# Optimization experiments

Measured on AMD Instinct MI355X. Metric: run time of the kernel, lower is better.

The kernel has to match this reference:

```python
import jax, jax.numpy as jnp
import numpy as np

N_NODES = 100000
N_EDGES = 1600000
IN_DIM = 128      # 1 (degree) + 127 (raw feat)
HID = 128
N_GRAPHS = 100


def setup_inputs() -> dict:
    key = jax.random.key(0)
    ks = jax.random.split(key, 16)
    feat = jax.random.normal(ks[0], (N_NODES, IN_DIM - 1), dtype=jnp.float32)
    src = jax.random.randint(ks[1], (N_EDGES,), 0, N_NODES, dtype=jnp.int32)
    dst = jax.random.randint(ks[2], (N_EDGES,), 0, N_NODES, dtype=jnp.int32)
    graph_ids = jnp.sort(jax.random.randint(ks[3], (N_NODES,), 0, N_GRAPHS, dtype=jnp.int32))
    s = 1.0 / np.sqrt(IN_DIM)
    W0 = jax.random.uniform(ks[4], (HID, IN_DIM), jnp.float32, -s, s)
    b0 = jax.random.uniform(ks[5], (HID,), jnp.float32, -s, s)
    s = 1.0 / np.sqrt(HID)
    W1 = jax.random.uniform(ks[6], (HID, HID), jnp.float32, -s, s)
    b1 = jax.random.uniform(ks[7], (HID,), jnp.float32, -s, s)
    W2 = jax.random.uniform(ks[8], (HID, HID), jnp.float32, -s, s)
    b2 = jax.random.uniform(ks[9], (HID,), jnp.float32, -s, s)
    Wc1 = jax.random.uniform(ks[10], (HID, HID), jnp.float32, -s, s)
    bc1 = jax.random.uniform(ks[11], (HID,), jnp.float32, -s, s)
    Wc2 = jax.random.uniform(ks[12], (1, HID), jnp.float32, -s, s)
    bc2 = jax.random.uniform(ks[13], (1,), jnp.float32, -s, s)
    return {"feat": feat, "src": src, "dst": dst, "graph_ids": graph_ids,
            "num_graphs": N_GRAPHS,
            "W0": W0, "b0": b0, "W1": W1, "b1": b1, "W2": W2, "b2": b2,
            "Wc1": Wc1, "bc1": bc1, "Wc2": Wc2, "bc2": bc2}


def _gcn_layer(h, src, dst, deg, W, b):
    # mean over in-neighbor messages; zero-in-degree nodes keep old h (DGL reduce never fires)
    n = h.shape[0]
    summed = jax.ops.segment_sum(h[src], dst, num_segments=n)  # [N, d]
    mean = summed / jnp.maximum(deg, 1.0)[:, None]
    agg = jnp.where((deg > 0)[:, None], mean, h)
    return jax.nn.relu(agg @ W.T + b)


def reference(feat, src, dst, graph_ids, num_graphs,
              W0, b0, W1, b1, W2, b2, Wc1, bc1, Wc2, bc2):
    n = feat.shape[0]
    deg = jax.ops.segment_sum(jnp.ones(src.shape[0], jnp.float32), dst, num_segments=n)  # in-degrees
    h = jnp.concatenate([deg[:, None], feat], axis=-1)  # [N, IN_DIM]
    for W, b in ((W0, b0), (W1, b1), (W2, b2)):
        h = _gcn_layer(h, src, dst, deg, W, b)
    # dgl.mean_nodes: per-graph mean of node features
    counts = jax.ops.segment_sum(jnp.ones(n, jnp.float32), graph_ids, num_segments=num_graphs)
    hg = jax.ops.segment_sum(h, graph_ids, num_segments=num_graphs) / jnp.maximum(counts, 1.0)[:, None]
    # faithful: classify1 applied twice, no activation (F.relu was passed as bias flag)
    hg = hg @ Wc1.T + bc1
    hg = hg @ Wc1.T + bc1
    hg = hg @ Wc2.T + bc2
    return hg  # [num_graphs, 1]
```

## Files before the change

### kernel.cpp

```cpp
#include <hip/hip_runtime.h>
#include <hip/hip_bf16.h>

#define HID 128
#define NRAW 127
#define BSH 8
#define BNODES 256
#define APAD 68


typedef __attribute__((ext_vector_type(8))) short short8;
typedef __attribute__((ext_vector_type(4))) float floatx4;
typedef __attribute__((ext_vector_type(2))) float floatx2;

__device__ inline unsigned pack_bf2(float x, float y) {
    unsigned bx = __float_as_uint(x);
    unsigned by = __float_as_uint(y);
    bx += 0x7fffu + ((bx >> 16) & 1u);
    by += 0x7fffu + ((by >> 16) & 1u);
    return (bx >> 16) | (by & 0xffff0000u);
}
__device__ inline float bf_lo(unsigned u) { return __uint_as_float(u << 16); }
__device__ inline float bf_hi(unsigned u) { return __uint_as_float(u & 0xffff0000u); }


__global__ void init_kernel(const float* __restrict__ W0, const float* __restrict__ W1,
                            const float* __restrict__ W2, const float* __restrict__ Wc1,
                            unsigned* __restrict__ O0, unsigned* __restrict__ O1,
                            unsigned* __restrict__ O2, float* __restrict__ Wc1p,
                            int* __restrict__ gbucket, float* __restrict__ hg,
                            float* __restrict__ counts, int G) {
    int id = blockIdx.x * blockDim.x + threadIdx.x;
    if (id < 512) gbucket[id] = 0;
    if (id < G * HID) hg[id] = 0.f;
    if (id < G) counts[id] = 0.f;
    if (id < 16384) {
        int t = id >> 7, p = id & 127;
        Wc1p[id] = Wc1[t * 128 + ((p & 7) * 16 + (p >> 3))];
    }
    if (id < 3 * 8192) {
        int sel = id >> 13, l = id & 8191;
        const float* W = sel == 0 ? W0 : (sel == 1 ? W1 : W2);
        unsigned* O = sel == 0 ? O0 : (sel == 1 ? O1 : O2);
        int o = l >> 6, pp = (l & 63) * 2;
        int k0 = (pp & 7) * 16 + (pp >> 3);
        int k1 = ((pp + 1) & 7) * 16 + ((pp + 1) >> 3);
        O[l] = pack_bf2(W[o * 128 + k0], W[o * 128 + k1]);
    }
}


__global__ __launch_bounds__(256) void bucket_count_kernel(const int* __restrict__ dst,
                                                           int* __restrict__ gbucket,
                                                           int E, int NB) {
    __shared__ int hist[512];
    int t = threadIdx.x;
    for (int b = t; b < NB; b += 256) hist[b] = 0;
    __syncthreads();
    int base = blockIdx.x * 4096;
    #pragma unroll
    for (int j = 0; j < 16; ++j) {
        int e = base + j * 256 + t;
        if (e < E) atomicAdd(&hist[dst[e] >> BSH], 1);
    }
    __syncthreads();
    for (int b = t; b < NB; b += 256) {
        int v = hist[b];
        if (v) atomicAdd(&gbucket[b], v);
    }
}

__global__ void bucket_scan_kernel(const int* __restrict__ gbucket, int* __restrict__ bstart,
                                   int* __restrict__ gcur, int NB, int E) {
    __shared__ int sm[512];
    int t = threadIdx.x;
    int v = (t < NB) ? gbucket[t] : 0;
    sm[t] = v;
    __syncthreads();
    for (int off = 1; off < 512; off <<= 1) {
        int add = (t >= off) ? sm[t - off] : 0;
        __syncthreads();
        sm[t] += add;
        __syncthreads();
    }
    if (t < NB) {
        int ex = sm[t] - v;
        bstart[t] = ex;
        gcur[t] = ex;
    }
    if (t == 0) bstart[NB] = E;
}

__global__ __launch_bounds__(256) void bucket_scatter_kernel(const int* __restrict__ src,
                                                             const int* __restrict__ dst,
                                                             int* __restrict__ gcur,
                                                             uint2* __restrict__ staging,
                                                             int E, int NB) {
    __shared__ int hist[512];
    __shared__ int base[512];
    int t = threadIdx.x;
    for (int b = t; b < NB; b += 256) hist[b] = 0;
    __syncthreads();
    int s[16], d[16], r[16];
    int e0 = blockIdx.x * 4096;
    #pragma unroll
    for (int j = 0; j < 16; ++j) {
        int e = e0 + j * 256 + t;
        if (e < E) {
            s[j] = src[e];
            d[j] = dst[e];
            r[j] = atomicAdd(&hist[d[j] >> BSH], 1);
        } else d[j] = -1;
    }
    __syncthreads();
    for (int b = t; b < NB; b += 256) {
        int v = hist[b];
        base[b] = v ? atomicAdd(&gcur[b], v) : 0;
    }
    __syncthreads();
    #pragma unroll
    for (int j = 0; j < 16; ++j) {
        if (d[j] >= 0) {
            int b = d[j] >> BSH;
            staging[base[b] + r[j]] = make_uint2((unsigned)s[j], (unsigned)d[j]);
        }
    }
}

__global__ __launch_bounds__(256) void csr_build_kernel(const uint2* __restrict__ staging,
                                                        const int* __restrict__ bstart,
                                                        int* __restrict__ rp, int* __restrict__ csr,
                                                        float* __restrict__ degf,
                                                        int N, int E, int NB) {
    __shared__ int hist[256];
    __shared__ int sm[256];
    __shared__ int excl[256];
    __shared__ int cnt[256];
    int t = threadIdx.x;
    int b = blockIdx.x;
    int nbase = b << BSH;
    int s0 = bstart[b], e1 = bstart[b + 1];
    hist[t] = 0;
    __syncthreads();
    for (int i = s0 + t; i < e1; i += 256) {
        uint2 p = staging[i];
        atomicAdd(&hist[p.y & (BNODES - 1)], 1);
    }
    __syncthreads();
    int h = hist[t];
    sm[t] = h;
    __syncthreads();
    for (int off = 1; off < 256; off <<= 1) {
        int add = (t >= off) ? sm[t - off] : 0;
        __syncthreads();
        sm[t] += add;
        __syncthreads();
    }
    excl[t] = sm[t] - h;
    cnt[t] = 0;
    int n = nbase + t;
    if (n < N) {
        rp[n] = s0 + (sm[t] - h);
        degf[n] = (float)h;
    }
    if (b == NB - 1 && t == 0) rp[N] = E;
    __syncthreads();
    for (int i = s0 + t; i < e1; i += 256) {
        uint2 p = staging[i];
        int dl = p.y & (BNODES - 1);
        int pos = s0 + excl[dl] + atomicAdd(&cnt[dl], 1);
        csr[pos] = (int)p.x;
    }
}


__global__ void build_h0_kernel(const float* __restrict__ feat,
                                unsigned* __restrict__ h8, int N) {
    int id = blockIdx.x * blockDim.x + threadIdx.x;
    if (id >= N * 32) return;
    int n = id >> 5, c = id & 31;
    const float* fr = feat + (size_t)n * NRAW;
    int base = c >> 1, hb = (c & 1) * 4;
    float f[4];
    #pragma unroll
    for (int j = 0; j < 4; ++j) {
        int l = (hb + j) * 16 + base;
        f[j] = (l == 0) ? 0.f : fr[l - 1];
    }
    unsigned w = __builtin_amdgcn_cvt_pk_fp8_f32(f[0], f[1], 0, false);
    w = __builtin_amdgcn_cvt_pk_fp8_f32(f[2], f[3], w, true);
    h8[id] = w;
}


__global__ __launch_bounds__(256) void agg_fp8_kernel(const unsigned* __restrict__ h8,
                                                      unsigned* __restrict__ agg,
                                                      const int* __restrict__ rp,
                                                      const int* __restrict__ csr,
                                                      const float* __restrict__ degf, int N) {
    int t = threadIdx.x;
    int col = t & 15;
    int i = blockIdx.x * 16 + (t >> 4);
    if (i >= N) return;
    int start = rp[i], end = rp[i + 1];
    int deg = end - start;
    const uint2* h2 = (const uint2*)h8;
    if (deg == 0) {
        uint2 v = h2[(size_t)i * 16 + col];
        floatx2 l0 = __builtin_amdgcn_cvt_pk_f32_fp8(v.x, false);
        floatx2 h0 = __builtin_amdgcn_cvt_pk_f32_fp8(v.x, true);
        floatx2 l1 = __builtin_amdgcn_cvt_pk_f32_fp8(v.y, false);
        floatx2 h1 = __builtin_amdgcn_cvt_pk_f32_fp8(v.y, true);
        uint4 r;
        r.x = pack_bf2(l0[0], l0[1]);
        r.y = pack_bf2(h0[0], h0[1]);
        r.z = pack_bf2(l1[0], l1[1]);
        r.w = pack_bf2(h1[0], h1[1]);
        ((uint4*)agg)[(size_t)i * 16 + col] = r;
        return;
    }
    floatx2 a0 = {0.f, 0.f}, a1 = {0.f, 0.f}, a2 = {0.f, 0.f}, a3 = {0.f, 0.f};
    float dsum = 0.f;
    int p = start;
    for (; p + 4 <= end; p += 4) {
        int i0 = csr[p];
        int i1 = csr[p + 1];
        int i2 = csr[p + 2];
        int i3 = csr[p + 3];
        uint2 v0 = h2[(size_t)i0 * 16 + col];
        uint2 v1 = h2[(size_t)i1 * 16 + col];
        uint2 v2 = h2[(size_t)i2 * 16 + col];
        uint2 v3 = h2[(size_t)i3 * 16 + col];
        if (degf && col == 0) dsum += degf[i0] + degf[i1] + degf[i2] + degf[i3];
        a0 += __builtin_amdgcn_cvt_pk_f32_fp8(v0.x, false);
        a1 += __builtin_amdgcn_cvt_pk_f32_fp8(v0.x, true);
        a2 += __builtin_amdgcn_cvt_pk_f32_fp8(v0.y, false);
        a3 += __builtin_amdgcn_cvt_pk_f32_fp8(v0.y, true);
        a0 += __builtin_amdgcn_cvt_pk_f32_fp8(v1.x, false);
        a1 += __builtin_amdgcn_cvt_pk_f32_fp8(v1.x, true);
        a2 += __builtin_amdgcn_cvt_pk_f32_fp8(v1.y, false);
        a3 += __builtin_amdgcn_cvt_pk_f32_fp8(v1.y, true);
        a0 += __builtin_amdgcn_cvt_pk_f32_fp8(v2.x, false);
        a1 += __builtin_amdgcn_cvt_pk_f32_fp8(v2.x, true);
        a2 += __builtin_amdgcn_cvt_pk_f32_fp8(v2.y, false);
        a3 += __builtin_amdgcn_cvt_pk_f32_fp8(v2.y, true);
        a0 += __builtin_amdgcn_cvt_pk_f32_fp8(v3.x, false);
        a1 += __builtin_amdgcn_cvt_pk_f32_fp8(v3.x, true);
        a2 += __builtin_amdgcn_cvt_pk_f32_fp8(v3.y, false);
        a3 += __builtin_amdgcn_cvt_pk_f32_fp8(v3.y, true);
    }
    for (; p < end; ++p) {
        int i0 = csr[p];
        uint2 v0 = h2[(size_t)i0 * 16 + col];
        if (degf && col == 0) dsum += degf[i0];
        a0 += __builtin_amdgcn_cvt_pk_f32_fp8(v0.x, false);
        a1 += __builtin_amdgcn_cvt_pk_f32_fp8(v0.x, true);
        a2 += __builtin_amdgcn_cvt_pk_f32_fp8(v0.y, false);
        a3 += __builtin_amdgcn_cvt_pk_f32_fp8(v0.y, true);
    }
    if (degf && col == 0) a0[0] = dsum;
    float inv = 1.f / (float)deg;
    uint4 r;
    r.x = pack_bf2(a0[0] * inv, a0[1] * inv);
    r.y = pack_bf2(a1[0] * inv, a1[1] * inv);
    r.z = pack_bf2(a2[0] * inv, a2[1] * inv);
    r.w = pack_bf2(a3[0] * inv, a3[1] * inv);
    ((uint4*)agg)[(size_t)i * 16 + col] = r;
}


__global__ __launch_bounds__(256) void mfma_gemm_kernel(const unsigned* __restrict__ A,
                                                        unsigned* __restrict__ out8,
                                                        unsigned* __restrict__ outb,
                                                        const unsigned* __restrict__ Wb,
                                                        const float* __restrict__ bias, int N) {
    __shared__ unsigned Al[64 * APAD];
    int t = threadIdx.x;
    int n0 = blockIdx.x * 64;
    #pragma unroll
    for (int c = 0; c < 4; ++c) {
        int f = c * 256 + t;
        int row = f >> 4, c4 = f & 15;
        int n = n0 + row;
        uint4 v = make_uint4(0u, 0u, 0u, 0u);
        if (n < N) v = ((const uint4*)A)[(size_t)n * 16 + c4];
        *(uint4*)&Al[row * APAD + c4 * 4] = v;
    }
    __syncthreads();

    int wv = t >> 6, lane = t & 63;
    int m = lane & 15, q = lane >> 4;
    floatx4 acc[8];
    #pragma unroll
    for (int ot = 0; ot < 8; ++ot) acc[ot] = (floatx4)(0.f);

    #pragma unroll
    for (int kt = 0; kt < 4; ++kt) {
        short8 af = *(const short8*)&Al[(wv * 16 + m) * APAD + kt * 16 + q * 4];
        short8 bf[8];
        #pragma unroll
        for (int ot = 0; ot < 8; ++ot)
            bf[ot] = *(const short8*)&Wb[(ot * 16 + m) * 64 + kt * 16 + q * 4];
        #pragma unroll
        for (int ot = 0; ot < 8; ++ot)
            acc[ot] = __builtin_amdgcn_mfma_f32_16x16x32_bf16(af, bf[ot], acc[ot], 0, 0, 0);
    }

    float bv[8];
    #pragma unroll
    for (int ot = 0; ot < 8; ++ot) bv[ot] = bias[ot * 16 + m];

    #pragma unroll
    for (int r = 0; r < 4; ++r) {
        int n = n0 + wv * 16 + q * 4 + r;
        if (n < N) {
            float vv[8];
            #pragma unroll
            for (int ot = 0; ot < 8; ++ot) vv[ot] = fmaxf(acc[ot][r] + bv[ot], 0.f);
            if (out8) {
                unsigned w0 = __builtin_amdgcn_cvt_pk_fp8_f32(vv[0], vv[1], 0, false);
                w0 = __builtin_amdgcn_cvt_pk_fp8_f32(vv[2], vv[3], w0, true);
                unsigned w1 = __builtin_amdgcn_cvt_pk_fp8_f32(vv[4], vv[5], 0, false);
                w1 = __builtin_amdgcn_cvt_pk_fp8_f32(vv[6], vv[7], w1, true);
                ((uint2*)out8)[(size_t)n * 16 + m] = make_uint2(w0, w1);
            }
            if (outb) {
                uint4 w;
                w.x = pack_bf2(vv[0], vv[1]);
                w.y = pack_bf2(vv[2], vv[3]);
                w.z = pack_bf2(vv[4], vv[5]);
                w.w = pack_bf2(vv[6], vv[7]);
                ((uint4*)outb)[(size_t)n * 16 + m] = w;
            }
        }
    }
}


__global__ __launch_bounds__(256) void pool_kernel(const unsigned* __restrict__ h,
                                                   const int* __restrict__ gid,
                                                   float* __restrict__ hg,
                                                   float* __restrict__ counts, int N) {
    int c = threadIdx.x & 63;
    int q = threadIdx.x >> 6;
    int n0 = blockIdx.x * 64;
    int nend = min(n0 + 64, N);
    float ax = 0.f, ay = 0.f, cnt = 0.f;
    int cur = -1;
    for (int n = n0 + q; n < nend; n += 4) {
        int g = gid[n];
        if (g != cur) {
            if (cur >= 0) {
                atomicAdd(&hg[cur * HID + 2 * c], ax);
                atomicAdd(&hg[cur * HID + 2 * c + 1], ay);
                if (c == 0) atomicAdd(&counts[cur], cnt);
            }
            ax = ay = cnt = 0.f;
            cur = g;
        }
        unsigned v = h[(size_t)n * 64 + c];
        ax += bf_lo(v); ay += bf_hi(v);
        cnt += 1.f;
    }
    if (cur >= 0) {
        atomicAdd(&hg[cur * HID + 2 * c], ax);
        atomicAdd(&hg[cur * HID + 2 * c + 1], ay);
        if (c == 0) atomicAdd(&counts[cur], cnt);
    }
}


__global__ __launch_bounds__(128) void cls_fused_kernel(const float* __restrict__ hg,
                                                        const float* __restrict__ counts,
                                                        const float* __restrict__ Wc1p,
                                                        const float* __restrict__ Wc1,
                                                        const float* __restrict__ bc1,
                                                        const float* __restrict__ Wc2,
                                                        const float* __restrict__ bc2,
                                                        float* __restrict__ out, int G) {
    __shared__ float x[128];
    __shared__ float y[128];
    __shared__ float red[128];
    int g = blockIdx.x, t = threadIdx.x;
    float inv = 1.f / fmaxf(counts[g], 1.f);
    x[t] = hg[g * HID + t] * inv;
    __syncthreads();
    const float4* wp4 = (const float4*)(Wc1p + t * HID);
    float s = 0.f;
    #pragma unroll
    for (int k4 = 0; k4 < 32; ++k4) {
        float4 w = wp4[k4];
        s += x[k4 * 4] * w.x + x[k4 * 4 + 1] * w.y + x[k4 * 4 + 2] * w.z + x[k4 * 4 + 3] * w.w;
    }
    y[t] = s + bc1[t];
    __syncthreads();
    const float4* w4 = (const float4*)(Wc1 + t * HID);
    float s2 = 0.f;
    #pragma unroll
    for (int k4 = 0; k4 < 32; ++k4) {
        float4 w = w4[k4];
        s2 += y[k4 * 4] * w.x + y[k4 * 4 + 1] * w.y + y[k4 * 4 + 2] * w.z + y[k4 * 4 + 3] * w.w;
    }
    red[t] = (s2 + bc1[t]) * Wc2[t];
    __syncthreads();
    if (t < 64) {
        float r = red[t] + red[t + 64];
        #pragma unroll
        for (int off = 32; off > 0; off >>= 1) r += __shfl_down(r, off);
        if (t == 0) out[g] = r + bc2[0];
    }
}


extern "C" void kernel_launch(void* const* d_in, const int* in_sizes, int n_in,
                              void* d_out, int out_size, void* d_ws, size_t ws_size,
                              hipStream_t stream) {
    const float* feat = (const float*)d_in[0];
    const int* src    = (const int*)d_in[1];
    const int* dst    = (const int*)d_in[2];
    const int* gid    = (const int*)d_in[3];
    const float* W0  = (const float*)d_in[5];
    const float* b0  = (const float*)d_in[6];
    const float* W1  = (const float*)d_in[7];
    const float* b1  = (const float*)d_in[8];
    const float* W2  = (const float*)d_in[9];
    const float* b2  = (const float*)d_in[10];
    const float* Wc1 = (const float*)d_in[11];
    const float* bc1 = (const float*)d_in[12];
    const float* Wc2 = (const float*)d_in[13];
    const float* bc2 = (const float*)d_in[14];

    const int N = in_sizes[3];
    const int E = in_sizes[1];
    const int G = out_size;
    const int NB = (N + BNODES - 1) >> BSH;

    char* ws = (char*)d_ws;
    size_t off = 0;
    auto alloc = [&](size_t bytes) { void* p = ws + off; off += (bytes + 255) & ~size_t(255); return p; };
    unsigned* h8     = (unsigned*)alloc((size_t)N * 32 * 4);
    unsigned* hB     = (unsigned*)alloc((size_t)N * 64 * 4);
    unsigned* aggbuf = (unsigned*)alloc((size_t)N * 64 * 4);
    float* degf      = (float*)alloc((size_t)N * 4);
    uint2* staging   = (uint2*)alloc((size_t)E * 8);
    int* csr         = (int*)alloc((size_t)E * 4);
    int* rp          = (int*)alloc((size_t)(N + 1) * 4);
    int* gbucket     = (int*)alloc(512 * 4);
    int* bstart      = (int*)alloc(513 * 4);
    int* gcur        = (int*)alloc(512 * 4);
    unsigned* Wb0    = (unsigned*)alloc(8192 * 4);
    unsigned* Wb1    = (unsigned*)alloc(8192 * 4);
    unsigned* Wb2    = (unsigned*)alloc(8192 * 4);
    float* Wc1p      = (float*)alloc(16384 * 4);
    float* hg        = (float*)alloc((size_t)G * HID * 4);
    float* counts    = (float*)alloc((size_t)G * 4);

    init_kernel<<<96, 256, 0, stream>>>(W0, W1, W2, Wc1, Wb0, Wb1, Wb2, Wc1p,
                                        gbucket, hg, counts, G);

    int gE = (E + 4095) / 4096;
    bucket_count_kernel<<<gE, 256, 0, stream>>>(dst, gbucket, E, NB);
    bucket_scan_kernel<<<1, 512, 0, stream>>>(gbucket, bstart, gcur, NB, E);
    bucket_scatter_kernel<<<gE, 256, 0, stream>>>(src, dst, gcur, staging, E, NB);
    csr_build_kernel<<<NB, 256, 0, stream>>>(staging, bstart, rp, csr, degf, N, E, NB);

    build_h0_kernel<<<(N * 32 + 255) / 256, 256, 0, stream>>>(feat, h8, N);

    int agg_grid = (N + 15) / 16;
    int gemm_grid = (N + 63) / 64;

    agg_fp8_kernel<<<agg_grid, 256, 0, stream>>>(h8, aggbuf, rp, csr, degf, N);
    mfma_gemm_kernel<<<gemm_grid, 256, 0, stream>>>(aggbuf, h8, nullptr, Wb0, b0, N);

    agg_fp8_kernel<<<agg_grid, 256, 0, stream>>>(h8, aggbuf, rp, csr, nullptr, N);
    mfma_gemm_kernel<<<gemm_grid, 256, 0, stream>>>(aggbuf, h8, nullptr, Wb1, b1, N);

    agg_fp8_kernel<<<agg_grid, 256, 0, stream>>>(h8, aggbuf, rp, csr, nullptr, N);
    mfma_gemm_kernel<<<gemm_grid, 256, 0, stream>>>(aggbuf, nullptr, hB, Wb2, b2, N);

    pool_kernel<<<(N + 63) / 64, 256, 0, stream>>>(hB, gid, hg, counts, N);

    cls_fused_kernel<<<G, 128, 0, stream>>>(hg, counts, Wc1p, Wc1, bc1, Wc2, bc2,
                                            (float*)d_out, G);
}
```

Measured before the change: 431.7 us.

## Unroll gather by 8 with predication and load GEMM A fragments directly from global

The neighbour-aggregation loop now issues eight index and feature loads per iteration, using clamped indices and masking instead of a separate remainder loop, so more gather loads are in flight. The GEMM kernel drops its shared-memory staging of the A tile and the barrier, and each lane loads its MFMA fragment straight from global memory. The A loads no longer check n < N, so the last block may read past the end of the buffer unless it is padded. Masked lanes in the gather still issue loads, which costs extra bandwidth on low-degree nodes.

After: 435.9 us. No clear change (+1.0%).

```diff
diff --git a/kernel.cpp b/kernel.cpp
--- a/kernel.cpp
+++ b/kernel.cpp
@@ -5,7 +5,6 @@
 #define NRAW 127
 #define BSH 8
 #define BNODES 256
-#define APAD 68
 
 
 typedef __attribute__((ext_vector_type(8))) short short8;
@@ -220,42 +219,28 @@
     }
     floatx2 a0 = {0.f, 0.f}, a1 = {0.f, 0.f}, a2 = {0.f, 0.f}, a3 = {0.f, 0.f};
     float dsum = 0.f;
-    int p = start;
-    for (; p + 4 <= end; p += 4) {
-        int i0 = csr[p];
-        int i1 = csr[p + 1];
-        int i2 = csr[p + 2];
-        int i3 = csr[p + 3];
-        uint2 v0 = h2[(size_t)i0 * 16 + col];
-        uint2 v1 = h2[(size_t)i1 * 16 + col];
-        uint2 v2 = h2[(size_t)i2 * 16 + col];
-        uint2 v3 = h2[(size_t)i3 * 16 + col];
-        if (degf && col == 0) dsum += degf[i0] + degf[i1] + degf[i2] + degf[i3];
-        a0 += __builtin_amdgcn_cvt_pk_f32_fp8(v0.x, false);
-        a1 += __builtin_amdgcn_cvt_pk_f32_fp8(v0.x, true);
-        a2 += __builtin_amdgcn_cvt_pk_f32_fp8(v0.y, false);
-        a3 += __builtin_amdgcn_cvt_pk_f32_fp8(v0.y, true);
-        a0 += __builtin_amdgcn_cvt_pk_f32_fp8(v1.x, false);
-        a1 += __builtin_amdgcn_cvt_pk_f32_fp8(v1.x, true);
-        a2 += __builtin_amdgcn_cvt_pk_f32_fp8(v1.y, false);
-        a3 += __builtin_amdgcn_cvt_pk_f32_fp8(v1.y, true);
-        a0 += __builtin_amdgcn_cvt_pk_f32_fp8(v2.x, false);
-        a1 += __builtin_amdgcn_cvt_pk_f32_fp8(v2.x, true);
-        a2 += __builtin_amdgcn_cvt_pk_f32_fp8(v2.y, false);
-        a3 += __builtin_amdgcn_cvt_pk_f32_fp8(v2.y, true);
-        a0 += __builtin_amdgcn_cvt_pk_f32_fp8(v3.x, false);
-        a1 += __builtin_amdgcn_cvt_pk_f32_fp8(v3.x, true);
-        a2 += __builtin_amdgcn_cvt_pk_f32_fp8(v3.y, false);
-        a3 += __builtin_amdgcn_cvt_pk_f32_fp8(v3.y, true);
-    }
-    for (; p < end; ++p) {
-        int i0 = csr[p];
-        uint2 v0 = h2[(size_t)i0 * 16 + col];
-        if (degf && col == 0) dsum += degf[i0];
-        a0 += __builtin_amdgcn_cvt_pk_f32_fp8(v0.x, false);
-        a1 += __builtin_amdgcn_cvt_pk_f32_fp8(v0.x, true);
-        a2 += __builtin_amdgcn_cvt_pk_f32_fp8(v0.y, false);
-        a3 += __builtin_amdgcn_cvt_pk_f32_fp8(v0.y, true);
+    for (int p = start; p < end; p += 8) {
+        int idx[8];
+        uint2 v[8];
+        #pragma unroll
+        for (int j = 0; j < 8; ++j) idx[j] = csr[min(p + j, end - 1)];
+        #pragma unroll
+        for (int j = 0; j < 8; ++j) v[j] = h2[(size_t)idx[j] * 16 + col];
+        if (degf && col == 0) {
+            #pragma unroll
+            for (int j = 0; j < 8; ++j)
+                if (p + j < end) dsum += degf[idx[j]];
+        }
+        #pragma unroll
+        for (int j = 0; j < 8; ++j) {
+            bool ok = (p + j) < end;
+            unsigned vx = ok ? v[j].x : 0u;
+            unsigned vy = ok ? v[j].y : 0u;
+            a0 += __builtin_amdgcn_cvt_pk_f32_fp8(vx, false);
+            a1 += __builtin_amdgcn_cvt_pk_f32_fp8(vx, true);
+            a2 += __builtin_amdgcn_cvt_pk_f32_fp8(vy, false);
+            a3 += __builtin_amdgcn_cvt_pk_f32_fp8(vy, true);
+        }
     }
     if (degf && col == 0) a0[0] = dsum;
     float inv = 1.f / (float)deg;
@@ -273,29 +258,19 @@
                                                         unsigned* __restrict__ outb,
                                                         const unsigned* __restrict__ Wb,
                                                         const float* __restrict__ bias, int N) {
-    __shared__ unsigned Al[64 * APAD];
-    int t = threadIdx.x;
-    int n0 = blockIdx.x * 64;
-    #pragma unroll
-    for (int c = 0; c < 4; ++c) {
-        int f = c * 256 + t;
-        int row = f >> 4, c4 = f & 15;
-        int n = n0 + row;
-        uint4 v = make_uint4(0u, 0u, 0u, 0u);
-        if (n < N) v = ((const uint4*)A)[(size_t)n * 16 + c4];
-        *(uint4*)&Al[row * APAD + c4 * 4] = v;
-    }
-    __syncthreads();
-
+    int t = threadIdx.x;
     int wv = t >> 6, lane = t & 63;
     int m = lane & 15, q = lane >> 4;
+    int n0 = blockIdx.x * 64;
+    const unsigned* abase = A + (size_t)(n0 + wv * 16 + m) * 64 + q * 4;
+
     floatx4 acc[8];
     #pragma unroll
     for (int ot = 0; ot < 8; ++ot) acc[ot] = (floatx4)(0.f);
 
     #pragma unroll
     for (int kt = 0; kt < 4; ++kt) {
-        short8 af = *(const short8*)&Al[(wv * 16 + m) * APAD + kt * 16 + q * 4];
+        short8 af = *(const short8*)(abase + kt * 16);
         short8 bf[8];
         #pragma unroll
         for (int ot = 0; ot < 8; ++ot)
```
